# Kernel tuning notes

Hardware: AMD Instinct MI355X
Metric: run time of the kernel (lower is better)

The kernel has to match this reference:

```python
import jax, jax.numpy as jnp
import numpy as np

N = 50000      # nodes
E = 800000     # edges
D_DISC = 64
D_CONT = 13    # per-slice continuous features (39/3)
EMB = 256
HID = 512
SLOPE = 0.01   # torch leaky_relu default


def lrelu(x):
    return jax.nn.leaky_relu(x, SLOPE)


def gcn_conv(x, W, b, src, dst, n):
    """PyG GCNConv with add_self_loops=True (self loops appended by caller),
    symmetric normalization D^-1/2 A D^-1/2, bias."""
    x = x @ W                                   # [N, EMB]
    ones = jnp.ones(src.shape[0], x.dtype)
    deg = jax.ops.segment_sum(ones, dst, num_segments=n)   # in-degree incl self loop
    dinv = jax.lax.rsqrt(jnp.maximum(deg, 1e-12))
    norm = dinv[src] * dinv[dst]                # [E+N]
    out = jax.ops.segment_sum(x[src] * norm[:, None], dst, num_segments=n)
    return out + b


def setup_inputs() -> dict:
    key = jax.random.key(0)
    ks = jax.random.split(key, 24)
    def lin(k, fan_in, fan_out):
        bound = 1.0 / np.sqrt(fan_in)
        k1, k2 = jax.random.split(k)
        W = jax.random.uniform(k1, (fan_in, fan_out), jnp.float32, -bound, bound)
        b = jax.random.uniform(k2, (fan_out,), jnp.float32, -bound, bound)
        return W, b
    Wd, bd = lin(ks[0], D_DISC, EMB)
    Wc1, bc1 = lin(ks[1], D_CONT, EMB)
    Wc2, bc2 = lin(ks[2], D_CONT, EMB)
    Wg0, bg0 = lin(ks[3], D_DISC, EMB)
    Wg1, bg1 = lin(ks[4], EMB, EMB)
    Wg2, bg2 = lin(ks[5], EMB, EMB)
    Wf, bf = lin(ks[6], 4 * EMB, HID)
    Wl1, bl1 = lin(ks[7], HID, HID // 2)
    Wl2, bl2 = lin(ks[8], HID // 2, 1)
    discrete_x = jax.random.normal(ks[9], (N, D_DISC), jnp.float32)
    continous_x = jax.random.normal(ks[10], (N, 3 * D_CONT), jnp.float32)
    edge_index = jax.random.randint(ks[11], (2, E), 0, N, jnp.int64)
    return {
        'discrete_x': discrete_x, 'continous_x': continous_x,
        'Wd': Wd, 'bd': bd, 'Wc1': Wc1, 'bc1': bc1, 'Wc2': Wc2, 'bc2': bc2,
        'Wg0': Wg0, 'bg0': bg0, 'Wg1': Wg1, 'bg1': bg1, 'Wg2': Wg2, 'bg2': bg2,
        'Wf': Wf, 'bf': bf, 'Wl1': Wl1, 'bl1': bl1, 'Wl2': Wl2, 'bl2': bl2,
        'edge_index': edge_index,
    }


def reference(discrete_x, continous_x, Wd, bd, Wc1, bc1, Wc2, bc2,
              Wg0, bg0, Wg1, bg1, Wg2, bg2, Wf, bf, Wl1, bl1, Wl2, bl2,
              edge_index):
    n = discrete_x.shape[0]
    loop = jnp.arange(n, dtype=edge_index.dtype)
    src = jnp.concatenate([edge_index[0], loop])
    dst = jnp.concatenate([edge_index[1], loop])

    x_d = lrelu(discrete_x @ Wd + bd)
    x_c1 = lrelu(continous_x[:, :13] @ Wc1 + bc1)
    x_c2 = lrelu(continous_x[:, 13:26] @ Wc2 + bc2)
    x_g = lrelu(discrete_x @ Wg0 + bg0)
    x_g = lrelu(gcn_conv(x_g, Wg1, bg1, src, dst, n))
    x_g = lrelu(gcn_conv(x_g, Wg2, bg2, src, dst, n))

    h_ci = lrelu(jnp.concatenate([x_d, x_c1, x_c2, x_g], axis=1) @ Wf + bf)
    s = lrelu(h_ci @ Wl1 + bl1)
    # dropout: eval mode (training=False) -> identity
    s_ci = jax.nn.sigmoid((s @ Wl2 + bl2)).squeeze()
    return (s_ci, s_ci, s_ci, h_ci, h_ci)
```

## Files before the change

kernel.cpp:

```cpp
#include <hip/hip_runtime.h>
#include <math.h>

#define NNODES 50000
#define NEDGES 800000
#define EMB 256
#define HID 512


typedef __bf16 bf16x8 __attribute__((ext_vector_type(8)));
typedef float f32x4 __attribute__((ext_vector_type(4)));
typedef unsigned short us4v __attribute__((ext_vector_type(4)));
typedef unsigned short us8v __attribute__((ext_vector_type(8)));

__device__ __forceinline__ unsigned short f2bf(float x) {
    unsigned int u = __float_as_uint(x);
    u += 0x7FFF + ((u >> 16) & 1);
    return (unsigned short)(u >> 16);
}

__device__ __forceinline__ f32x4 mfma_bf16(us8v a, us8v b, f32x4 c) {
    return __builtin_amdgcn_mfma_f32_16x16x32_bf16(
        __builtin_bit_cast(bf16x8, a), __builtin_bit_cast(bf16x8, b), c, 0, 0, 0);
}

__global__ void wsplit(const float* __restrict__ W, int K, int N,
                       unsigned short* __restrict__ th, unsigned short* __restrict__ tl)
{
    int idx = blockIdx.x * 256 + threadIdx.x;
    if (idx >= K * N) return;
    int n = idx / K, k = idx - n * K;
    float x = W[(size_t)k * N + n];
    unsigned short h = f2bf(x);
    float hf = __uint_as_float((unsigned int)h << 16);
    th[idx] = h;
    tl[idx] = f2bf(x - hf);
}

__global__ __launch_bounds__(256) void gemm_mfma(
    const float* __restrict__ A, int lda,
    const unsigned short* __restrict__ BTh, const unsigned short* __restrict__ BTl,
    float* __restrict__ C, int ldc, float* __restrict__ C2,
    const float* __restrict__ bias, int M, int N, int K, int act)
{
    __shared__ unsigned short AsH[2][128 * 64];
    __shared__ unsigned short AsL[2][128 * 64];
    const int bm = blockIdx.y * 128;
    const int bn = blockIdx.x * 128;
    const int tid = threadIdx.x;
    const int lane = tid & 63;
    const int wid = tid >> 6;
    const int wm = wid >> 1, wn = wid & 1;
    const int l15 = lane & 15, l4 = lane >> 4;

    int smidx[8], sj4[8];
    const float* sptr[8];
#pragma unroll
    for (int u = 0; u < 8; ++u) {
        int fid = tid + u * 256;
        int m = fid >> 4;
        int j4 = fid & 15;
        smidx[u] = m;
        sj4[u] = j4;
        int gr = bm + m;
        sptr[u] = (gr < M) ? (A + (size_t)gr * lda + j4 * 4) : nullptr;
    }

    const unsigned short* bhp[4];
    const unsigned short* blp[4];
#pragma unroll
    for (int fj = 0; fj < 4; ++fj) {
        size_t coff = (size_t)(bn + wn * 64 + fj * 16 + l15) * (size_t)K;
        bhp[fj] = BTh + coff;
        blp[fj] = BTl + coff;
    }

    f32x4 acc[4][4] = {};
    float4 pref[8];

    const int nk = K >> 6;

#pragma unroll
    for (int u = 0; u < 8; ++u)
        pref[u] = sptr[u] ? *(const float4*)(sptr[u]) : make_float4(0.f, 0.f, 0.f, 0.f);

    for (int t = 0; t < nk; ++t) {
        const int cur = t & 1;
#pragma unroll
        for (int u = 0; u < 8; ++u) {
            float e[4] = {pref[u].x, pref[u].y, pref[u].z, pref[u].w};
            us4v h, l;
#pragma unroll
            for (int q = 0; q < 4; ++q) {
                unsigned short hh = f2bf(e[q]);
                h[q] = hh;
                l[q] = f2bf(e[q] - __uint_as_float((unsigned int)hh << 16));
            }
            int m = smidx[u], j4 = sj4[u];
            int phys = m * 64 + ((((j4 >> 1)) ^ (m & 7)) << 3) + (j4 & 1) * 4;
            *(us4v*)&AsH[cur][phys] = h;
            *(us4v*)&AsL[cur][phys] = l;
        }
        __syncthreads();

        if (t + 1 < nk) {
            const int koff = (t + 1) * 64;
#pragma unroll
            for (int u = 0; u < 8; ++u)
                pref[u] = sptr[u] ? *(const float4*)(sptr[u] + koff)
                                  : make_float4(0.f, 0.f, 0.f, 0.f);
        }

        const int k0 = t * 64;
#pragma unroll
        for (int ks = 0; ks < 2; ++ks) {
            us8v ah[4], al[4], bh[4], bl[4];
            const int kb = ks * 4 + l4;
#pragma unroll
            for (int fi = 0; fi < 4; ++fi) {
                int row = wm * 64 + fi * 16 + l15;
                int phys = row * 64 + ((kb ^ (row & 7)) << 3);
                ah[fi] = *(const us8v*)&AsH[cur][phys];
                al[fi] = *(const us8v*)&AsL[cur][phys];
            }
            const size_t kg = (size_t)(k0 + ks * 32 + l4 * 8);
#pragma unroll
            for (int fj = 0; fj < 4; ++fj) {
                bh[fj] = *(const us8v*)(bhp[fj] + kg);
                bl[fj] = *(const us8v*)(blp[fj] + kg);
            }
#pragma unroll
            for (int fj = 0; fj < 4; ++fj)
#pragma unroll
                for (int fi = 0; fi < 4; ++fi)
                    acc[fi][fj] = mfma_bf16(ah[fi], bh[fj], acc[fi][fj]);
#pragma unroll
            for (int fj = 0; fj < 4; ++fj)
#pragma unroll
                for (int fi = 0; fi < 4; ++fi)
                    acc[fi][fj] = mfma_bf16(al[fi], bh[fj], acc[fi][fj]);
#pragma unroll
            for (int fj = 0; fj < 4; ++fj)
#pragma unroll
                for (int fi = 0; fi < 4; ++fi)
                    acc[fi][fj] = mfma_bf16(ah[fi], bl[fj], acc[fi][fj]);
        }
    }

    float bs[4];
#pragma unroll
    for (int fj = 0; fj < 4; ++fj)
        bs[fj] = bias ? bias[bn + wn * 64 + fj * 16 + l15] : 0.f;

#pragma unroll
    for (int fi = 0; fi < 4; ++fi) {
#pragma unroll
        for (int r = 0; r < 4; ++r) {
            int row = bm + wm * 64 + fi * 16 + l4 * 4 + r;
            if (row >= M) continue;
#pragma unroll
            for (int fj = 0; fj < 4; ++fj) {
                int col = bn + wn * 64 + fj * 16 + l15;
                float v = acc[fi][fj][r] + bs[fj];
                if (act) v = v > 0.f ? v : 0.01f * v;
                C[(size_t)row * ldc + col] = v;
                if (C2) C2[(size_t)row * ldc + col] = v;
            }
        }
    }
}

#define BM 128
#define BN 128
#define BK 16

__global__ __launch_bounds__(256) void gemm_kernel(
    const float* __restrict__ A, int lda,
    const float* __restrict__ B, int ldb,
    float* __restrict__ C, int ldc,
    float* __restrict__ C2,
    const float* __restrict__ bias,
    int M, int N, int K, int act)
{
    __shared__ float As[BK][BM];
    __shared__ float Bs[BK][BN];
    const int bm = blockIdx.y * BM;
    const int bn = blockIdx.x * BN;
    const int tid = threadIdx.x;
    const int tx = tid & 15;
    const int ty = tid >> 4;

    const bool avec = ((((uintptr_t)A) & 15) == 0) && ((lda & 3) == 0);

    float acc[8][8] = {};

    for (int k0 = 0; k0 < K; k0 += BK) {
        if (avec) {
#pragma unroll
            for (int it = 0; it < 2; ++it) {
                int aid = tid + it * 256;
                int m = aid >> 2;
                int kq = aid & 3;
                int gr = bm + m;
                int gk = k0 + kq * 4;
                float4 v = {0.f, 0.f, 0.f, 0.f};
                if (gr < M) {
                    if (gk + 3 < K) {
                        v = *(const float4*)(A + (size_t)gr * lda + gk);
                    } else {
                        float t0 = (gk + 0 < K) ? A[(size_t)gr * lda + gk + 0] : 0.f;
                        float t1 = (gk + 1 < K) ? A[(size_t)gr * lda + gk + 1] : 0.f;
                        float t2 = (gk + 2 < K) ? A[(size_t)gr * lda + gk + 2] : 0.f;
                        float t3 = (gk + 3 < K) ? A[(size_t)gr * lda + gk + 3] : 0.f;
                        v = make_float4(t0, t1, t2, t3);
                    }
                }
                int k = kq * 4;
                As[k + 0][m ^ (((k + 0) & 7) << 2)] = v.x;
                As[k + 1][m ^ (((k + 1) & 7) << 2)] = v.y;
                As[k + 2][m ^ (((k + 2) & 7) << 2)] = v.z;
                As[k + 3][m ^ (((k + 3) & 7) << 2)] = v.w;
            }
        } else {
            for (int l = tid; l < BM * BK; l += 256) {
                int m = l >> 4;
                int k = l & 15;
                int gr = bm + m, gc = k0 + k;
                float v = (gr < M && gc < K) ? A[(size_t)gr * lda + gc] : 0.f;
                As[k][m ^ ((k & 7) << 2)] = v;
            }
        }
#pragma unroll
        for (int it = 0; it < 2; ++it) {
            int fid = tid + it * 256;
            int k = fid >> 5;
            int n4 = fid & 31;
            int gk = k0 + k;
            int gn = bn + n4 * 4;
            float4 v = {0.f, 0.f, 0.f, 0.f};
            if (gk < K) {
                if (gn + 3 < N) {
                    v = *(const float4*)(B + (size_t)gk * ldb + gn);
                } else {
                    float t0 = (gn + 0 < N) ? B[(size_t)gk * ldb + gn + 0] : 0.f;
                    float t1 = (gn + 1 < N) ? B[(size_t)gk * ldb + gn + 1] : 0.f;
                    float t2 = (gn + 2 < N) ? B[(size_t)gk * ldb + gn + 2] : 0.f;
                    float t3 = (gn + 3 < N) ? B[(size_t)gk * ldb + gn + 3] : 0.f;
                    v = make_float4(t0, t1, t2, t3);
                }
            }
            *(float4*)&Bs[k][n4 * 4] = v;
        }
        __syncthreads();

#pragma unroll
        for (int k = 0; k < BK; ++k) {
            const int sw = (k & 7) << 2;
            float4 a0 = *(const float4*)&As[k][(ty * 4) ^ sw];
            float4 a1 = *(const float4*)&As[k][(ty * 4 + 64) ^ sw];
            float4 b0 = *(const float4*)&Bs[k][tx * 4];
            float4 b1 = *(const float4*)&Bs[k][tx * 4 + 64];
            float av[8] = {a0.x, a0.y, a0.z, a0.w, a1.x, a1.y, a1.z, a1.w};
            float bv[8] = {b0.x, b0.y, b0.z, b0.w, b1.x, b1.y, b1.z, b1.w};
#pragma unroll
            for (int i = 0; i < 8; ++i)
#pragma unroll
                for (int j = 0; j < 8; ++j)
                    acc[i][j] += av[i] * bv[j];
        }
        __syncthreads();
    }

#pragma unroll
    for (int i = 0; i < 8; ++i) {
        int r = bm + ((i >> 2) * 64) + ty * 4 + (i & 3);
        if (r >= M) continue;
#pragma unroll
        for (int jh = 0; jh < 2; ++jh) {
            int c0 = bn + jh * 64 + tx * 4;
            if (c0 + 3 < N) {
                float v0 = acc[i][jh * 4 + 0];
                float v1 = acc[i][jh * 4 + 1];
                float v2 = acc[i][jh * 4 + 2];
                float v3 = acc[i][jh * 4 + 3];
                if (bias) {
                    v0 += bias[c0 + 0]; v1 += bias[c0 + 1];
                    v2 += bias[c0 + 2]; v3 += bias[c0 + 3];
                }
                if (act) {
                    v0 = v0 > 0.f ? v0 : 0.01f * v0;
                    v1 = v1 > 0.f ? v1 : 0.01f * v1;
                    v2 = v2 > 0.f ? v2 : 0.01f * v2;
                    v3 = v3 > 0.f ? v3 : 0.01f * v3;
                }
                float4 pack = make_float4(v0, v1, v2, v3);
                *(float4*)(C + (size_t)r * ldc + c0) = pack;
                if (C2) *(float4*)(C2 + (size_t)r * ldc + c0) = pack;
            } else {
#pragma unroll
                for (int e = 0; e < 4; ++e) {
                    int c = c0 + e;
                    if (c >= N) continue;
                    float v = acc[i][jh * 4 + e];
                    if (bias) v += bias[c];
                    if (act) v = v > 0.f ? v : 0.01f * v;
                    C[(size_t)r * ldc + c] = v;
                    if (C2) C2[(size_t)r * ldc + c] = v;
                }
            }
        }
    }
}

__global__ void count_deg(const int* __restrict__ dst, int* __restrict__ deg, int nE)
{
    int e = blockIdx.x * 256 + threadIdx.x;
    if (e < nE) atomicAdd(&deg[dst[e]], 1);
}

__global__ void dinv_kernel(const int* __restrict__ deg, float* __restrict__ dinv, int n)
{
    int i = blockIdx.x * 256 + threadIdx.x;
    if (i < n) dinv[i] = rsqrtf((float)deg[i] + 1.0f);
}

__global__ __launch_bounds__(256) void scan1(const int* __restrict__ deg,
                                             int* __restrict__ excl,
                                             int* __restrict__ blocksum, int n)
{
    __shared__ int tsum[256];
    int base = blockIdx.x * 1024;
    int t = threadIdx.x;
    int v[4], s = 0;
#pragma unroll
    for (int j = 0; j < 4; ++j) {
        int idx = base + t * 4 + j;
        v[j] = (idx < n) ? deg[idx] : 0;
        s += v[j];
    }
    tsum[t] = s;
    __syncthreads();
    for (int off = 1; off < 256; off <<= 1) {
        int x = (t >= off) ? tsum[t - off] : 0;
        __syncthreads();
        tsum[t] += x;
        __syncthreads();
    }
    int toff = tsum[t] - s;
    int run = 0;
#pragma unroll
    for (int j = 0; j < 4; ++j) {
        int idx = base + t * 4 + j;
        if (idx < n) excl[idx] = toff + run;
        run += v[j];
    }
    if (t == 255) blocksum[blockIdx.x] = tsum[255];
}

__global__ void scan2(int* __restrict__ blocksum, int nb)
{
    if (threadIdx.x == 0 && blockIdx.x == 0) {
        int run = 0;
        for (int i = 0; i < nb; ++i) {
            int v = blocksum[i];
            blocksum[i] = run;
            run += v;
        }
    }
}

__global__ void scan3(int* __restrict__ rowptr, int* __restrict__ cursor,
                      const int* __restrict__ excl, const int* __restrict__ blocksum, int n)
{
    int idx = blockIdx.x * 256 + threadIdx.x;
    if (idx < n) {
        int v = excl[idx] + blocksum[idx >> 10];
        rowptr[idx] = v;
        cursor[idx] = v;
    }
    if (idx == 0) rowptr[n] = NEDGES;
}

__global__ void fill_csr(const int* __restrict__ src, const int* __restrict__ dst,
                         const float* __restrict__ dinv, int* __restrict__ cursor,
                         int* __restrict__ src_sorted, float* __restrict__ w_sorted, int nE)
{
    int e = blockIdx.x * 256 + threadIdx.x;
    if (e >= nE) return;
    int s = src[e], d = dst[e];
    int pos = atomicAdd(&cursor[d], 1);
    src_sorted[pos] = s;
    w_sorted[pos] = dinv[s] * dinv[d];
}

__global__ __launch_bounds__(256) void gather_conv(
    const float* __restrict__ t, const int* __restrict__ rowptr,
    const int* __restrict__ src_sorted, const float* __restrict__ w_sorted,
    const float* __restrict__ dinv, const float* __restrict__ bias,
    float* __restrict__ out, int ldc)
{
    int node = blockIdx.x * 4 + (threadIdx.x >> 6);
    if (node >= NNODES) return;
    int lane = threadIdx.x & 63;
    int p0 = rowptr[node], p1 = rowptr[node + 1];
    const float4* tv = (const float4*)t;
    float4 acc = {0.f, 0.f, 0.f, 0.f};
    for (int p = p0; p < p1; ++p) {
        int s = src_sorted[p];
        float w = w_sorted[p];
        float4 v = tv[(size_t)s * 64 + lane];
        acc.x += v.x * w; acc.y += v.y * w; acc.z += v.z * w; acc.w += v.w * w;
    }
    float di = dinv[node];
    float w2 = di * di;
    float4 self = tv[(size_t)node * 64 + lane];
    float4 b = ((const float4*)bias)[lane];
    acc.x += self.x * w2 + b.x;
    acc.y += self.y * w2 + b.y;
    acc.z += self.z * w2 + b.z;
    acc.w += self.w * w2 + b.w;
    acc.x = acc.x > 0.f ? acc.x : 0.01f * acc.x;
    acc.y = acc.y > 0.f ? acc.y : 0.01f * acc.y;
    acc.z = acc.z > 0.f ? acc.z : 0.01f * acc.z;
    acc.w = acc.w > 0.f ? acc.w : 0.01f * acc.w;
    *((float4*)(out + (size_t)node * ldc) + lane) = acc;
}

__global__ __launch_bounds__(256) void rowdot_sigmoid(
    const float* __restrict__ s, const float* __restrict__ w, const float* __restrict__ b,
    float* __restrict__ out, int n)
{
    int row = blockIdx.x * 4 + (threadIdx.x >> 6);
    int lane = threadIdx.x & 63;
    if (row >= n) return;
    const float4* sr = (const float4*)(s + (size_t)row * 256);
    const float4* wr = (const float4*)w;
    float4 a = sr[lane], c = wr[lane];
    float p = a.x * c.x + a.y * c.y + a.z * c.z + a.w * c.w;
#pragma unroll
    for (int off = 32; off > 0; off >>= 1) p += __shfl_down(p, off);
    if (lane == 0) {
        float v = 1.0f / (1.0f + expf(-(p + b[0])));
        out[row] = v;
        out[n + row] = v;
        out[2 * n + row] = v;
    }
}

extern "C" void kernel_launch(void* const* d_in, const int* in_sizes, int n_in,
                              void* d_out, int out_size, void* d_ws, size_t ws_size,
                              hipStream_t stream)
{
    const float* discrete_x = (const float*)d_in[0];
    const float* continous_x = (const float*)d_in[1];
    const float* Wd  = (const float*)d_in[2];  const float* bd  = (const float*)d_in[3];
    const float* Wc1 = (const float*)d_in[4];  const float* bc1 = (const float*)d_in[5];
    const float* Wc2 = (const float*)d_in[6];  const float* bc2 = (const float*)d_in[7];
    const float* Wg0 = (const float*)d_in[8];  const float* bg0 = (const float*)d_in[9];
    const float* Wg1 = (const float*)d_in[10]; const float* bg1 = (const float*)d_in[11];
    const float* Wg2 = (const float*)d_in[12]; const float* bg2 = (const float*)d_in[13];
    const float* Wf  = (const float*)d_in[14]; const float* bf  = (const float*)d_in[15];
    const float* Wl1 = (const float*)d_in[16]; const float* bl1 = (const float*)d_in[17];
    const float* Wl2 = (const float*)d_in[18]; const float* bl2 = (const float*)d_in[19];
    const int* edge_index = (const int*)d_in[20];
    const int* src = edge_index;
    const int* dst = edge_index + NEDGES;

    float* out = (float*)d_out;
    float* ws = (float*)d_ws;

    float* dinv       = ws;
    int*   deg        = (int*)(ws + 50048);
    int*   rowptr     = (int*)(ws + 2 * 50048);
    int*   cursor     = (int*)(ws + 3 * 50048 + 64);
    int*   excl       = (int*)(ws + 4 * 50048 + 64);
    int*   blocksum   = (int*)(ws + 5 * 50048 + 64);
    int*   src_sorted = (int*)(ws + 5 * 50048 + 128);
    float* w_sorted   = ws + 5 * 50048 + 128 + NEDGES;
    float* xcat       = w_sorted + NEDGES;
    float* xg         = xcat + (size_t)NNODES * 1024;
    float* tbuf       = xg   + (size_t)NNODES * EMB;
    float* sbuf       = tbuf + (size_t)NNODES * EMB;

    float* h_out  = out + 3 * (size_t)NNODES;
    float* h_out2 = h_out + (size_t)NNODES * HID;

    unsigned short* wl1_h = (unsigned short*)out;
    unsigned short* wl1_l = wl1_h + 512 * 256;
    unsigned short* wd_h  = (unsigned short*)h_out2;
    unsigned short* wd_l  = wd_h  + 64 * 256;
    unsigned short* wg0_h = wd_l  + 64 * 256;
    unsigned short* wg0_l = wg0_h + 64 * 256;
    unsigned short* wg1_h = wg0_l + 64 * 256;
    unsigned short* wg1_l = wg1_h + 256 * 256;
    unsigned short* wg2_h = wg1_l + 256 * 256;
    unsigned short* wg2_l = wg2_h + 256 * 256;
    unsigned short* wf_h  = (unsigned short*)sbuf;
    unsigned short* wf_l  = wf_h + 1024 * 512;

    dim3 blk(256);
    auto gemmF = [&](const float* A, int lda, const float* B, int ldb, float* C, int ldc,
                     float* C2, const float* bias, int M, int N, int K, int act) {
        dim3 grid((N + BN - 1) / BN, (M + BM - 1) / BM);
        hipLaunchKernelGGL(gemm_kernel, grid, blk, 0, stream,
                           A, lda, B, ldb, C, ldc, C2, bias, M, N, K, act);
    };
    auto gemmM = [&](const float* A, int lda, const unsigned short* th, const unsigned short* tl,
                     float* C, int ldc, float* C2, const float* bias,
                     int M, int N, int K, int act) {
        dim3 grid(N / 128, (M + 127) / 128);
        hipLaunchKernelGGL(gemm_mfma, grid, blk, 0, stream,
                           A, lda, th, tl, C, ldc, C2, bias, M, N, K, act);
    };
    auto wsp = [&](const float* W, int K, int N, unsigned short* th, unsigned short* tl) {
        hipLaunchKernelGGL(wsplit, dim3((K * N + 255) / 256), blk, 0, stream, W, K, N, th, tl);
    };

    wsp(Wd,  64,   256, wd_h,  wd_l);
    wsp(Wg0, 64,   256, wg0_h, wg0_l);
    wsp(Wg1, 256,  256, wg1_h, wg1_l);
    wsp(Wg2, 256,  256, wg2_h, wg2_l);
    wsp(Wf,  1024, 512, wf_h,  wf_l);
    wsp(Wl1, 512,  256, wl1_h, wl1_l);

    hipMemsetAsync(deg, 0, NNODES * sizeof(int), stream);
    hipLaunchKernelGGL(count_deg, dim3((NEDGES + 255) / 256), blk, 0, stream, dst, deg, NEDGES);
    hipLaunchKernelGGL(dinv_kernel, dim3((NNODES + 255) / 256), blk, 0, stream, deg, dinv, NNODES);
    int nb = (NNODES + 1023) / 1024;
    hipLaunchKernelGGL(scan1, dim3(nb), blk, 0, stream, deg, excl, blocksum, NNODES);
    hipLaunchKernelGGL(scan2, dim3(1), blk, 0, stream, blocksum, nb);
    hipLaunchKernelGGL(scan3, dim3((NNODES + 255) / 256), blk, 0, stream,
                       rowptr, cursor, excl, blocksum, NNODES);
    hipLaunchKernelGGL(fill_csr, dim3((NEDGES + 255) / 256), blk, 0, stream,
                       src, dst, dinv, cursor, src_sorted, w_sorted, NEDGES);

    gemmM(discrete_x, 64, wd_h, wd_l, xcat + 0, 1024, nullptr, bd, NNODES, 256, 64, 1);
    gemmF(continous_x,      39, Wc1, EMB, xcat + 256, 1024, nullptr, bc1, NNODES, EMB, 13, 1);
    gemmF(continous_x + 13, 39, Wc2, EMB, xcat + 512, 1024, nullptr, bc2, NNODES, EMB, 13, 1);
    gemmM(discrete_x, 64, wg0_h, wg0_l, xg, EMB, nullptr, bg0, NNODES, 256, 64, 1);

    gemmM(xg, EMB, wg1_h, wg1_l, tbuf, EMB, nullptr, nullptr, NNODES, 256, 256, 0);
    hipLaunchKernelGGL(gather_conv, dim3((NNODES + 3) / 4), blk, 0, stream,
                       tbuf, rowptr, src_sorted, w_sorted, dinv, bg1, xg, EMB);

    gemmM(xg, EMB, wg2_h, wg2_l, tbuf, EMB, nullptr, nullptr, NNODES, 256, 256, 0);
    hipLaunchKernelGGL(gather_conv, dim3((NNODES + 3) / 4), blk, 0, stream,
                       tbuf, rowptr, src_sorted, w_sorted, dinv, bg2, xcat + 768, 1024);

    gemmM(xcat, 1024, wf_h, wf_l, h_out, HID, h_out2, bf, NNODES, 512, 1024, 1);

    gemmM(h_out, HID, wl1_h, wl1_l, sbuf, 256, nullptr, bl1, NNODES, 256, 512, 1);

    hipLaunchKernelGGL(rowdot_sigmoid, dim3((NNODES + 3) / 4), blk, 0, stream,
                       sbuf, Wl2, bl2, out, NNODES);
}
```

Measured before the change: 1.316 ms.

## Store activations pre-split into bf16 hi/lo and stream A tiles via global_load_lds

Producer kernels (the small GEMMs, the fallback GEMM and gather_conv) now write their activations as separate bf16 high and low planes instead of fp32. A new MFMA GEMM variant reads these planes and copies A tiles straight into swizzled LDS with global_load_lds double buffering. This removes the per-tile fp32-to-bf16 split and the register staging from the main GEMM loops; discrete_x is split once up front. Total bytes moved stay about the same. Rows past M in the last tile are loaded without a bounds guard, and the fallback GEMM epilogue loses its vectorized float4 store.

```diff
diff --git a/kernel.cpp b/kernel.cpp
--- a/kernel.cpp
+++ b/kernel.cpp
@@ -21,6 +21,12 @@
 __device__ __forceinline__ f32x4 mfma_bf16(us8v a, us8v b, f32x4 c) {
     return __builtin_amdgcn_mfma_f32_16x16x32_bf16(
         __builtin_bit_cast(bf16x8, a), __builtin_bit_cast(bf16x8, b), c, 0, 0, 0);
+}
+
+__device__ __forceinline__ void gl16(const unsigned short* g, unsigned short* l) {
+    __builtin_amdgcn_global_load_lds(
+        (const __attribute__((address_space(1))) unsigned int*)g,
+        (__attribute__((address_space(3))) unsigned int*)l, 16, 0, 0);
 }
 
 __global__ void wsplit(const float* __restrict__ W, int K, int N,
@@ -36,10 +42,22 @@
     tl[idx] = f2bf(x - hf);
 }
 
-__global__ __launch_bounds__(256) void gemm_mfma(
-    const float* __restrict__ A, int lda,
+__global__ void xsplit(const float* __restrict__ X, int n,
+                       unsigned short* __restrict__ xh, unsigned short* __restrict__ xl)
+{
+    int i = blockIdx.x * 256 + threadIdx.x;
+    if (i >= n) return;
+    float x = X[i];
+    unsigned short h = f2bf(x);
+    xh[i] = h;
+    xl[i] = f2bf(x - __uint_as_float((unsigned int)h << 16));
+}
+
+__global__ __launch_bounds__(256) void gemm_mfma_p(
+    const unsigned short* __restrict__ Ah, const unsigned short* __restrict__ Al, int lda,
     const unsigned short* __restrict__ BTh, const unsigned short* __restrict__ BTl,
     float* __restrict__ C, int ldc, float* __restrict__ C2,
+    unsigned short* __restrict__ Ch, unsigned short* __restrict__ Cl, int ldcp,
     const float* __restrict__ bias, int M, int N, int K, int act)
 {
     __shared__ unsigned short AsH[2][128 * 64];
@@ -52,6 +70,137 @@
     const int wm = wid >> 1, wn = wid & 1;
     const int l15 = lane & 15, l4 = lane >> 4;
 
+    const int rg = lane >> 3;
+    const int sb = (lane & 7) ^ rg;
+    size_t soff[4];
+#pragma unroll
+    for (int i = 0; i < 4; ++i) {
+        int g = wid * 4 + i;
+        soff[i] = (size_t)(bm + g * 8 + rg) * (size_t)lda + (size_t)(sb * 8);
+    }
+
+    const unsigned short* bhp[4];
+    const unsigned short* blp[4];
+#pragma unroll
+    for (int fj = 0; fj < 4; ++fj) {
+        size_t coff = (size_t)(bn + wn * 64 + fj * 16 + l15) * (size_t)K;
+        bhp[fj] = BTh + coff;
+        blp[fj] = BTl + coff;
+    }
+
+    f32x4 acc[4][4] = {};
+    const int nk = K >> 6;
+
+#pragma unroll
+    for (int i = 0; i < 4; ++i) {
+        int g = wid * 4 + i;
+        gl16(Ah + soff[i], &AsH[0][g * 512]);
+        gl16(Al + soff[i], &AsL[0][g * 512]);
+    }
+    __syncthreads();
+
+    for (int t = 0; t < nk; ++t) {
+        const int cur = t & 1;
+        const int k0 = t * 64;
+
+        us8v bh[2][4], bl[2][4];
+#pragma unroll
+        for (int ks = 0; ks < 2; ++ks) {
+            const size_t kg = (size_t)(k0 + ks * 32 + l4 * 8);
+#pragma unroll
+            for (int fj = 0; fj < 4; ++fj) {
+                bh[ks][fj] = *(const us8v*)(bhp[fj] + kg);
+                bl[ks][fj] = *(const us8v*)(blp[fj] + kg);
+            }
+        }
+
+        if (t + 1 < nk) {
+            const size_t ko = (size_t)(k0 + 64);
+#pragma unroll
+            for (int i = 0; i < 4; ++i) {
+                int g = wid * 4 + i;
+                gl16(Ah + soff[i] + ko, &AsH[cur ^ 1][g * 512]);
+                gl16(Al + soff[i] + ko, &AsL[cur ^ 1][g * 512]);
+            }
+        }
+
+#pragma unroll
+        for (int ks = 0; ks < 2; ++ks) {
+            us8v ah[4], al[4];
+            const int kb = ks * 4 + l4;
+#pragma unroll
+            for (int fi = 0; fi < 4; ++fi) {
+                int row = wm * 64 + fi * 16 + l15;
+                int phys = row * 64 + ((kb ^ (row & 7)) << 3);
+                ah[fi] = *(const us8v*)&AsH[cur][phys];
+                al[fi] = *(const us8v*)&AsL[cur][phys];
+            }
+#pragma unroll
+            for (int fj = 0; fj < 4; ++fj)
+#pragma unroll
+                for (int fi = 0; fi < 4; ++fi)
+                    acc[fi][fj] = mfma_bf16(ah[fi], bh[ks][fj], acc[fi][fj]);
+#pragma unroll
+            for (int fj = 0; fj < 4; ++fj)
+#pragma unroll
+                for (int fi = 0; fi < 4; ++fi)
+                    acc[fi][fj] = mfma_bf16(al[fi], bh[ks][fj], acc[fi][fj]);
+#pragma unroll
+            for (int fj = 0; fj < 4; ++fj)
+#pragma unroll
+                for (int fi = 0; fi < 4; ++fi)
+                    acc[fi][fj] = mfma_bf16(ah[fi], bl[ks][fj], acc[fi][fj]);
+        }
+        __syncthreads();
+    }
+
+    float bs[4];
+#pragma unroll
+    for (int fj = 0; fj < 4; ++fj)
+        bs[fj] = bias ? bias[bn + wn * 64 + fj * 16 + l15] : 0.f;
+
+#pragma unroll
+    for (int fi = 0; fi < 4; ++fi) {
+#pragma unroll
+        for (int r = 0; r < 4; ++r) {
+            int row = bm + wm * 64 + fi * 16 + l4 * 4 + r;
+            if (row >= M) continue;
+#pragma unroll
+            for (int fj = 0; fj < 4; ++fj) {
+                int col = bn + wn * 64 + fj * 16 + l15;
+                float v = acc[fi][fj][r] + bs[fj];
+                if (act) v = v > 0.f ? v : 0.01f * v;
+                if (C) {
+                    C[(size_t)row * ldc + col] = v;
+                    if (C2) C2[(size_t)row * ldc + col] = v;
+                }
+                if (Ch) {
+                    unsigned short h = f2bf(v);
+                    Ch[(size_t)row * ldcp + col] = h;
+                    Cl[(size_t)row * ldcp + col] =
+                        f2bf(v - __uint_as_float((unsigned int)h << 16));
+                }
+            }
+        }
+    }
+}
+
+__global__ __launch_bounds__(256) void gemm_mfma(
+    const float* __restrict__ A, int lda,
+    const unsigned short* __restrict__ BTh, const unsigned short* __restrict__ BTl,
+    float* __restrict__ C, int ldc, float* __restrict__ C2,
+    const float* __restrict__ bias, int M, int N, int K, int act)
+{
+    __shared__ unsigned short AsH[2][128 * 64];
+    __shared__ unsigned short AsL[2][128 * 64];
+    const int bm = blockIdx.y * 128;
+    const int bn = blockIdx.x * 128;
+    const int tid = threadIdx.x;
+    const int lane = tid & 63;
+    const int wid = tid >> 6;
+    const int wm = wid >> 1, wn = wid & 1;
+    const int l15 = lane & 15, l4 = lane >> 4;
+
     int smidx[8], sj4[8];
     const float* sptr[8];
 #pragma unroll
@@ -76,7 +225,6 @@
 
     f32x4 acc[4][4] = {};
     float4 pref[8];
-
     const int nk = K >> 6;
 
 #pragma unroll
@@ -178,6 +326,7 @@
     const float* __restrict__ B, int ldb,
     float* __restrict__ C, int ldc,
     float* __restrict__ C2,
+    unsigned short* __restrict__ Ch, unsigned short* __restrict__ Cl, int ldcp,
     const float* __restrict__ bias,
     int M, int N, int K, int act)
 {
@@ -277,32 +426,19 @@
 #pragma unroll
         for (int jh = 0; jh < 2; ++jh) {
             int c0 = bn + jh * 64 + tx * 4;
-            if (c0 + 3 < N) {
-                float v0 = acc[i][jh * 4 + 0];
-                float v1 = acc[i][jh * 4 + 1];
-                float v2 = acc[i][jh * 4 + 2];
-                float v3 = acc[i][jh * 4 + 3];
-                if (bias) {
-                    v0 += bias[c0 + 0]; v1 += bias[c0 + 1];
-                    v2 += bias[c0 + 2]; v3 += bias[c0 + 3];
-                }
-                if (act) {
-                    v0 = v0 > 0.f ? v0 : 0.01f * v0;
-                    v1 = v1 > 0.f ? v1 : 0.01f * v1;
-                    v2 = v2 > 0.f ? v2 : 0.01f * v2;
-                    v3 = v3 > 0.f ? v3 : 0.01f * v3;
-                }
-                float4 pack = make_float4(v0, v1, v2, v3);
-                *(float4*)(C + (size_t)r * ldc + c0) = pack;
-                if (C2) *(float4*)(C2 + (size_t)r * ldc + c0) = pack;
-            } else {
-#pragma unroll
-                for (int e = 0; e < 4; ++e) {
-                    int c = c0 + e;
-                    if (c >= N) continue;
-                    float v = acc[i][jh * 4 + e];
-                    if (bias) v += bias[c];
-                    if (act) v = v > 0.f ? v : 0.01f * v;
+#pragma unroll
+            for (int e = 0; e < 4; ++e) {
+                int c = c0 + e;
+                if (c >= N) continue;
+                float v = acc[i][jh * 4 + e];
+                if (bias) v += bias[c];
+                if (act) v = v > 0.f ? v : 0.01f * v;
+                if (Ch) {
+                    unsigned short h = f2bf(v);
+                    Ch[(size_t)r * ldcp + c] = h;
+                    Cl[(size_t)r * ldcp + c] =
+                        f2bf(v - __uint_as_float((unsigned int)h << 16));
+                } else {
                     C[(size_t)r * ldc + c] = v;
                     if (C2) C2[(size_t)r * ldc + c] = v;
                 }
@@ -396,7 +532,7 @@
     const float* __restrict__ t, const int* __restrict__ rowptr,
     const int* __restrict__ src_sorted, const float* __restrict__ w_sorted,
     const float* __restrict__ dinv, const float* __restrict__ bias,
-    float* __restrict__ out, int ldc)
+    unsigned short* __restrict__ oh, unsigned short* __restrict__ ol, int ldcp)
 {
     int node = blockIdx.x * 4 + (threadIdx.x >> 6);
     if (node >= NNODES) return;
@@ -414,15 +550,21 @@
     float w2 = di * di;
     float4 self = tv[(size_t)node * 64 + lane];
     float4 b = ((const float4*)bias)[lane];
-    acc.x += self.x * w2 + b.x;
-    acc.y += self.y * w2 + b.y;
-    acc.z += self.z * w2 + b.z;
-    acc.w += self.w * w2 + b.w;
-    acc.x = acc.x > 0.f ? acc.x : 0.01f * acc.x;
-    acc.y = acc.y > 0.f ? acc.y : 0.01f * acc.y;
-    acc.z = acc.z > 0.f ? acc.z : 0.01f * acc.z;
-    acc.w = acc.w > 0.f ? acc.w : 0.01f * acc.w;
-    *((float4*)(out + (size_t)node * ldc) + lane) = acc;
+    float e[4];
+    e[0] = acc.x + self.x * w2 + b.x;
+    e[1] = acc.y + self.y * w2 + b.y;
+    e[2] = acc.z + self.z * w2 + b.z;
+    e[3] = acc.w + self.w * w2 + b.w;
+    us4v h4, l4v;
+#pragma unroll
+    for (int q = 0; q < 4; ++q) {
+        float v = e[q] > 0.f ? e[q] : 0.01f * e[q];
+        unsigned short h = f2bf(v);
+        h4[q] = h;
+        l4v[q] = f2bf(v - __uint_as_float((unsigned int)h << 16));
+    }
+    *(us4v*)(oh + (size_t)node * ldcp + lane * 4) = h4;
+    *(us4v*)(ol + (size_t)node * ldcp + lane * 4) = l4v;
 }
 
 __global__ __launch_bounds__(256) void rowdot_sigmoid(
@@ -484,6 +626,11 @@
     float* h_out  = out + 3 * (size_t)NNODES;
     float* h_out2 = h_out + (size_t)NNODES * HID;
 
+    unsigned short* xcat_h = (unsigned short*)xcat;
+    unsigned short* xcat_l = xcat_h + (size_t)NNODES * 1024;
+    unsigned short* xg_h   = (unsigned short*)xg;
+    unsigned short* xg_l   = xg_h + (size_t)NNODES * 256;
+
     unsigned short* wl1_h = (unsigned short*)out;
     unsigned short* wl1_l = wl1_h + 512 * 256;
     unsigned short* wd_h  = (unsigned short*)h_out2;
@@ -496,20 +643,27 @@
     unsigned short* wg2_l = wg2_h + 256 * 256;
     unsigned short* wf_h  = (unsigned short*)sbuf;
     unsigned short* wf_l  = wf_h + 1024 * 512;
+    unsigned short* dx_h  = wf_l + 1024 * 512;
+    unsigned short* dx_l  = dx_h + (size_t)NNODES * 64;
 
     dim3 blk(256);
-    auto gemmF = [&](const float* A, int lda, const float* B, int ldb, float* C, int ldc,
-                     float* C2, const float* bias, int M, int N, int K, int act) {
+    auto gemmF = [&](const float* A, int lda, const float* B, int ldb,
+                     unsigned short* ch, unsigned short* cl, int ldcp,
+                     const float* bias, int M, int N, int K, int act) {
         dim3 grid((N + BN - 1) / BN, (M + BM - 1) / BM);
         hipLaunchKernelGGL(gemm_kernel, grid, blk, 0, stream,
-                           A, lda, B, ldb, C, ldc, C2, bias, M, N, K, act);
+                           A, lda, B, ldb, (float*)nullptr, 0, (float*)nullptr,
+                           ch, cl, ldcp, bias, M, N, K, act);
     };
-    auto gemmM = [&](const float* A, int lda, const unsigned short* th, const unsigned short* tl,
-                     float* C, int ldc, float* C2, const float* bias,
-                     int M, int N, int K, int act) {
+    auto gemmP = [&](const unsigned short* ah, const unsigned short* al, int lda,
+                     const unsigned short* th, const unsigned short* tl,
+                     float* Cf, int ldc, float* C2,
+                     unsigned short* ch, unsigned short* cl, int ldcp,
+                     const float* bias, int M, int N, int K, int act) {
         dim3 grid(N / 128, (M + 127) / 128);
-        hipLaunchKernelGGL(gemm_mfma, grid, blk, 0, stream,
-                           A, lda, th, tl, C, ldc, C2, bias, M, N, K, act);
+        hipLaunchKernelGGL(gemm_mfma_p, grid, blk, 0, stream,
+                           ah, al, lda, th, tl, Cf, ldc, C2, ch, cl, ldcp,
+                           bias, M, N, K, act);
     };
     auto wsp = [&](const float* W, int K, int N, unsigned short* th, unsigned short* tl) {
         hipLaunchKernelGGL(wsplit, dim3((K * N + 255) / 256), blk, 0, stream, W, K, N, th, tl);
@@ -521,6 +675,8 @@
     wsp(Wg2, 256,  256, wg2_h, wg2_l);
     wsp(Wf,  1024, 512, wf_h,  wf_l);
     wsp(Wl1, 512,  256, wl1_h, wl1_l);
+    hipLaunchKernelGGL(xsplit, dim3((NNODES * 64 + 255) / 256), blk, 0, stream,
+                       discrete_x, NNODES * 64, dx_h, dx_l);
 
     hipMemsetAsync(deg, 0, NNODES * sizeof(int), stream);
     hipLaunchKernelGGL(count_deg, dim3((NEDGES + 255) / 256), blk, 0, stream, dst, deg, NEDGES);
@@ -533,22 +689,35 @@
     hipLaunchKernelGGL(fill_csr, dim3((NEDGES + 255) / 256), blk, 0, stream,
                        src, dst, dinv, cursor, src_sorted, w_sorted, NEDGES);
 
-    gemmM(discrete_x, 64, wd_h, wd_l, xcat + 0, 1024, nullptr, bd, NNODES, 256, 64, 1);
-    gemmF(continous_x,      39, Wc1, EMB, xcat + 256, 1024, nullptr, bc1, NNODES, EMB, 13, 1);
-    gemmF(continous_x + 13, 39, Wc2, EMB, xcat + 512, 1024, nullptr, bc2, NNODES, EMB, 13, 1);
-    gemmM(discrete_x, 64, wg0_h, wg0_l, xg, EMB, nullptr, bg0, NNODES, 256, 64, 1);
-
-    gemmM(xg, EMB, wg1_h, wg1_l, tbuf, EMB, nullptr, nullptr, NNODES, 256, 256, 0);
+    gemmP(dx_h, dx_l, 64, wd_h, wd_l, nullptr, 0, nullptr,
+          xcat_h, xcat_l, 1024, bd, NNODES, 256, 64, 1);
+    gemmF(continous_x,      39, Wc1, EMB, xcat_h + 256, xcat_l + 256, 1024,
+          bc1, NNODES, EMB, 13, 1);
+    gemmF(continous_x + 13, 39, Wc2, EMB, xcat_h + 512, xcat_l + 512, 1024,
+          bc2, NNODES, EMB, 13, 1);
+    gemmP(dx_h, dx_l, 64, wg0_h, wg0_l, nullptr, 0, nullptr,
+          xg_h, xg_l, 256, bg0, NNODES, 256, 64, 1);
+
+    gemmP(xg_h, xg_l, 256, wg1_h, wg1_l, tbuf, 256, nullptr,
+          nullptr, nullptr, 0, nullptr, NNODES, 256, 256, 0);
     hipLaunchKernelGGL(gather_conv, dim3((NNODES + 3) / 4), blk, 0, stream,
-                       tbuf, rowptr, src_sorted, w_sorted, dinv, bg1, xg, EMB);
-
-    gemmM(xg, EMB, wg2_h, wg2_l, tbuf, EMB, nullptr, nullptr, NNODES, 256, 256, 0);
+                       tbuf, rowptr, src_sorted, w_sorted, dinv, bg1, xg_h, xg_l, 256);
+
+    gemmP(xg_h, xg_l, 256, wg2_h, wg2_l, tbuf, 256, nullptr,
+          nullptr, nullptr, 0, nullptr, NNODES, 256, 256, 0);
     hipLaunchKernelGGL(gather_conv, dim3((NNODES + 3) / 4), blk, 0, stream,
-                       tbuf, rowptr, src_sorted, w_sorted, dinv, bg2, xcat + 768, 1024);
-
-    gemmM(xcat, 1024, wf_h, wf_l, h_out, HID, h_out2, bf, NNODES, 512, 1024, 1);
-
-    gemmM(h_out, HID, wl1_h, wl1_l, sbuf, 256, nullptr, bl1, NNODES, 256, 512, 1);
+                       tbuf, rowptr, src_sorted, w_sorted, dinv, bg2,
+                       xcat_h + 768, xcat_l + 768, 1024);
+
+    gemmP(xcat_h, xcat_l, 1024, wf_h, wf_l, h_out, HID, h_out2,
+          nullptr, nullptr, 0, bf, NNODES, 512, 1024, 1);
+
+    {
+        dim3 grid(256 / 128, (NNODES + 127) / 128);
+        hipLaunchKernelGGL(gemm_mfma, grid, blk, 0, stream,
+                           h_out, HID, wl1_h, wl1_l, sbuf, 256, (float*)nullptr,
+                           bl1, NNODES, 256, 512, 1);
+    }
 
     hipLaunchKernelGGL(rowdot_sigmoid, dim3((NNODES + 3) / 4), blk, 0, stream,
                        sbuf, Wl2, bl2, out, NNODES);
```

Result: no change. 1.302 ms (-1.1%).
